# Optimization experiments

Hardware: AMD Instinct MI355X
Metric: run time of the kernel (lower is better)

The kernel has to match this reference:

```python
import jax, jax.numpy as jnp
import numpy as np

B, T, D, H = 4, 2048, 1024, 16
HD = D // H  # head_size = 64


def setup_inputs() -> dict:
    key = jax.random.key(0)
    ks = jax.random.split(key, 6)
    s = 0.02
    x = jax.random.normal(ks[0], (B, T, D), dtype=jnp.float32)
    # per-head unfused projections, stacked over heads: [H, D, HD]
    Wq = jax.random.normal(ks[1], (H, D, HD), dtype=jnp.float32) * s
    Wk = jax.random.normal(ks[2], (H, D, HD), dtype=jnp.float32) * s
    Wv = jax.random.normal(ks[3], (H, D, HD), dtype=jnp.float32) * s
    # output projection, torch Linear layout [out, in]
    Wo = jax.random.normal(ks[4], (D, D), dtype=jnp.float32) * s
    bo = jax.random.normal(ks[5], (D,), dtype=jnp.float32) * s
    return {"x": x, "Wq": Wq, "Wk": Wk, "Wv": Wv, "Wo": Wo, "bo": bo}


def reference(x, Wq, Wk, Wv, Wo, bo):
    b, t, d = x.shape
    hd = Wq.shape[-1]
    q = jnp.einsum('btd,hdk->bhtk', x, Wq)
    k = jnp.einsum('btd,hdk->bhtk', x, Wk)
    v = jnp.einsum('btd,hdk->bhtk', x, Wv)
    scores = jnp.einsum('bhtk,bhsk->bhts', q, k) / jnp.sqrt(jnp.float32(hd))
    mask = jnp.tril(jnp.ones((t, t), dtype=bool))  # causal
    scores = jnp.where(mask, scores, jnp.float32(-jnp.inf))
    p = jax.nn.softmax(scores, axis=-1)
    o = jnp.einsum('bhts,bhsk->bhtk', p, v)
    o = o.transpose(0, 2, 1, 3).reshape(b, t, d)  # concat heads
    return o @ Wo.T + bo
```

## Files before the change

kernel.cpp:

```cpp
#include <hip/hip_runtime.h>
#include <hip/hip_bf16.h>
#include <stdint.h>

#define B_   4
#define T_   2048
#define D_   1024
#define H_   16
#define HD_  64
#define MROWS (B_*T_)
#define NQKV  3072
#define NST  (T_/64)

typedef __attribute__((ext_vector_type(8))) short  short8;
typedef __attribute__((ext_vector_type(4))) short  bf16x4;
typedef __attribute__((ext_vector_type(4))) float  floatx4;

#define QSCALE 0.1803368801111244f

__device__ inline void async_copy16(const __hip_bfloat16* g, __hip_bfloat16* l) {
  __builtin_amdgcn_global_load_lds(
      (const __attribute__((address_space(1))) void*)g,
      (__attribute__((address_space(3))) void*)l, 16, 0, 0);
}

__device__ inline floatx4 mfma16(bf16x4 a, bf16x4 b, floatx4 c) {
#if __has_builtin(__builtin_amdgcn_mfma_f32_16x16x16bf16_1k)
  return __builtin_amdgcn_mfma_f32_16x16x16bf16_1k(a, b, c, 0, 0, 0);
#elif __has_builtin(__builtin_amdgcn_mfma_f32_16x16x16_bf16)
  return __builtin_amdgcn_mfma_f32_16x16x16_bf16(a, b, c, 0, 0, 0);
#else
  short8 a8 = (short8){a[0], a[1], a[2], a[3], 0, 0, 0, 0};
  short8 b8 = (short8){b[0], b[1], b[2], b[3], 0, 0, 0, 0};
  return __builtin_amdgcn_mfma_f32_16x16x32_bf16(a8, b8, c, 0, 0, 0);
#endif
}

__global__ void prep(const float* __restrict__ x, const float* __restrict__ Wo,
                     const float* __restrict__ Wq, const float* __restrict__ Wk,
                     const float* __restrict__ Wv,
                     __hip_bfloat16* __restrict__ xb, __hip_bfloat16* __restrict__ wob,
                     __hip_bfloat16* __restrict__ wqkv) {
  __shared__ __hip_bfloat16 tile[64][65];
  const int bid = (int)blockIdx.x;
  const int t = threadIdx.x;
  if (bid < 8192) {
    int i = (bid * 256 + t) * 4;
    float4 v = *(const float4*)(x + i);
    xb[i + 0] = __float2bfloat16(v.x);
    xb[i + 1] = __float2bfloat16(v.y);
    xb[i + 2] = __float2bfloat16(v.z);
    xb[i + 3] = __float2bfloat16(v.w);
  } else if (bid < 9216) {
    int i = ((bid - 8192) * 256 + t) * 4;
    float4 v = *(const float4*)(Wo + i);
    wob[i + 0] = __float2bfloat16(v.x);
    wob[i + 1] = __float2bfloat16(v.y);
    wob[i + 2] = __float2bfloat16(v.z);
    wob[i + 3] = __float2bfloat16(v.w);
  } else {
    int idx = bid - 9216;
    const int d0 = (idx & 15) * 64;
    const int wh = idx >> 4;
    const int which = wh >> 4, h = wh & 15;
    const float* W = (which == 0) ? Wq : ((which == 1) ? Wk : Wv);
    const float* base = W + (size_t)h * D_ * HD_;
#pragma unroll
    for (int i = 0; i < 16; i++) {
      int e = i * 256 + t;
      int dr = e >> 6, hd = e & 63;
      tile[dr][hd] = __float2bfloat16(base[(size_t)(d0 + dr) * HD_ + hd]);
    }
    __syncthreads();
#pragma unroll
    for (int i = 0; i < 16; i++) {
      int e = i * 256 + t;
      int hd = e >> 6, dr = e & 63;
      wqkv[(size_t)(which * 1024 + h * 64 + hd) * D_ + d0 + dr] = tile[dr][hd];
    }
  }
}

__global__ void repack_kv(const __hip_bfloat16* __restrict__ qkv,
                          __hip_bfloat16* __restrict__ kpack, __hip_bfloat16* __restrict__ vpack) {
  __shared__ __hip_bfloat16 Ks[64][72];
  __shared__ __hip_bfloat16 Vs[64][72];
  const int tid = threadIdx.x;
  const int st = blockIdx.x, bh = blockIdx.y;
  const int b = bh >> 4, h = bh & 15;
#pragma unroll
  for (int p = 0; p < 2; p++) {
    int c = p * 256 + tid;
    int row = c >> 3, col8 = c & 7;
    const __hip_bfloat16* src = qkv + (size_t)(b * T_ + st * 64 + row) * NQKV + h * HD_ + col8 * 8;
    *(uint4*)&Ks[row][col8 * 8] = *(const uint4*)(src + 1024);
    *(uint4*)&Vs[row][col8 * 8] = *(const uint4*)(src + 2048);
  }
  __syncthreads();
  const size_t base = ((size_t)bh * NST + st) * 8 * 512;
#pragma unroll
  for (int p = 0; p < 2; p++) {
    int pair = p * 256 + tid;
    int c = pair >> 6, l = pair & 63;
    int lq = l & 15, q = l >> 4;
    int ni = c >> 1, half = c & 1;
    short8 v = *(const short8*)&Ks[ni * 16 + lq][half * 32 + q * 8];
    *(short8*)(kpack + base + (size_t)c * 512 + l * 8) = v;
  }
#pragma unroll
  for (int p = 0; p < 2; p++) {
    int pair = p * 256 + tid;
    int c = pair >> 6, l = pair & 63;
    int lq = l & 15, q = l >> 4;
    int m = c >> 2, nt = c & 3;
    __hip_bfloat16 tmp[8];
#pragma unroll
    for (int half = 0; half < 2; half++)
#pragma unroll
      for (int j = 0; j < 4; j++)
        tmp[half * 4 + j] = Vs[(2 * m + half) * 16 + q * 4 + j][nt * 16 + lq];
    *(short8*)(vpack + base + (size_t)c * 512 + l * 8) = *(short8*)tmp;
  }
}

template <int EPI>
__launch_bounds__(256, 2)
__global__ void gemm_bt(const __hip_bfloat16* __restrict__ A, const __hip_bfloat16* __restrict__ Bt,
                        __hip_bfloat16* __restrict__ Cb, float* __restrict__ Cf,
                        const float* __restrict__ bias, int M, int N, int K, float qscale) {
  __shared__ __hip_bfloat16 As[128 * 32];
  __shared__ __hip_bfloat16 Bs[128 * 32];
  const int tid = threadIdx.x;
  const int w = tid >> 6, lane = tid & 63;
  const int lq = lane & 15, quad = lane >> 4;
  const int wr = w >> 1, wc = w & 1;
  const int m0 = blockIdx.x * 128, n0 = blockIdx.y * 128;

  floatx4 acc[4][4];
#pragma unroll
  for (int i = 0; i < 4; i++)
#pragma unroll
    for (int j = 0; j < 4; j++) acc[i][j] = (floatx4){0.f, 0.f, 0.f, 0.f};

  for (int k0 = 0; k0 < K; k0 += 32) {
    __syncthreads();
#pragma unroll
    for (int ph = 0; ph < 2; ++ph) {
      int c = ph * 256 + tid;
      int row = c >> 2, col8 = c & 3;
      async_copy16(A + (size_t)(m0 + row) * K + k0 + col8 * 8, As + c * 8);
      async_copy16(Bt + (size_t)(n0 + row) * K + k0 + col8 * 8, Bs + c * 8);
    }
    __syncthreads();
    short8 af[4], bf[4];
#pragma unroll
    for (int mi = 0; mi < 4; mi++)
      af[mi] = *(const short8*)(As + (wr * 64 + mi * 16 + lq) * 32 + quad * 8);
#pragma unroll
    for (int ni = 0; ni < 4; ni++)
      bf[ni] = *(const short8*)(Bs + (wc * 64 + ni * 16 + lq) * 32 + quad * 8);
#pragma unroll
    for (int mi = 0; mi < 4; mi++)
#pragma unroll
      for (int ni = 0; ni < 4; ni++)
        acc[mi][ni] = __builtin_amdgcn_mfma_f32_16x16x32_bf16(af[mi], bf[ni], acc[mi][ni], 0, 0, 0);
  }

#pragma unroll
  for (int mi = 0; mi < 4; mi++) {
#pragma unroll
    for (int ni = 0; ni < 4; ni++) {
      int col = n0 + wc * 64 + ni * 16 + lq;
      if (EPI == 0) {
        float s = (col < 1024) ? qscale : 1.0f;
#pragma unroll
        for (int r = 0; r < 4; r++) {
          int row = m0 + wr * 64 + mi * 16 + quad * 4 + r;
          Cb[(size_t)row * N + col] = __float2bfloat16(acc[mi][ni][r] * s);
        }
      } else {
        float bv = bias[col];
#pragma unroll
        for (int r = 0; r < 4; r++) {
          int row = m0 + wr * 64 + mi * 16 + quad * 4 + r;
          Cf[(size_t)row * N + col] = acc[mi][ni][r] + bv;
        }
      }
    }
  }
}

__launch_bounds__(256, 2)
__global__ void attn(const __hip_bfloat16* __restrict__ qkv,
                     const __hip_bfloat16* __restrict__ kpack,
                     const __hip_bfloat16* __restrict__ vpack,
                     __hip_bfloat16* __restrict__ obuf) {
  __shared__ __hip_bfloat16 KVs[2][8192];
  const int tid = threadIdx.x;
  const int w = tid >> 6, lane = tid & 63;
  const int lq = lane & 15, quad = lane >> 4;

  const int bh = (int)blockIdx.x;
  const int a  = (int)blockIdx.y;
  const int b = bh >> 4, h = bh & 15;

  const __hip_bfloat16* kbase = kpack + ((size_t)bh * NST) * 4096;
  const __hip_bfloat16* vbase = vpack + ((size_t)bh * NST) * 4096;

#pragma unroll 1
  for (int seg = 0; seg < 2; ++seg) {
    const int tbase = seg ? (NST - 2 - 2 * a) : (2 * a);
    const int qt = tbase + (w >> 1);
    const int rbase = (w & 1) * 32;

    short8 qf[2][2];
#pragma unroll
    for (int bi = 0; bi < 2; bi++) {
      const __hip_bfloat16* qp =
          qkv + ((size_t)(b * T_ + qt * 64 + rbase + bi * 16 + lq)) * NQKV + h * HD_;
      qf[bi][0] = *(const short8*)(qp + quad * 8);
      qf[bi][1] = *(const short8*)(qp + 32 + quad * 8);
    }

    floatx4 Oacc[2][4];
#pragma unroll
    for (int bi = 0; bi < 2; bi++)
#pragma unroll
      for (int i = 0; i < 4; i++) Oacc[bi][i] = (floatx4){0.f, 0.f, 0.f, 0.f};
    float lrow[2] = {0.f, 0.f};

    const int itTop = tbase + 1;

#pragma unroll
    for (int j = 0; j < 2; ++j) {
      int c = j * 256 + tid;
      async_copy16(kbase + (size_t)c * 8, &KVs[0][0] + c * 8);
      async_copy16(vbase + (size_t)c * 8, &KVs[0][4096] + c * 8);
    }
    __syncthreads();

#pragma unroll 1
    for (int it = 0; it <= itTop; ++it) {
      const int cur = it & 1;
      if (it < itTop) {
        const __hip_bfloat16* kn = kbase + (size_t)(it + 1) * 4096;
        const __hip_bfloat16* vn = vbase + (size_t)(it + 1) * 4096;
#pragma unroll
        for (int j = 0; j < 2; ++j) {
          int c = j * 256 + tid;
          async_copy16(kn + (size_t)c * 8, &KVs[cur ^ 1][0] + c * 8);
          async_copy16(vn + (size_t)c * 8, &KVs[cur ^ 1][4096] + c * 8);
        }
      }
      if (it <= qt) {
        const __hip_bfloat16* Kb = &KVs[cur][0] + lane * 8;
        const __hip_bfloat16* Vb = &KVs[cur][4096] + lane * 8;
        short8 kf[4], kg[4];
#pragma unroll
        for (int ni = 0; ni < 4; ni++) {
          kf[ni] = *(const short8*)(Kb + (size_t)(ni * 2 + 0) * 512);
          kg[ni] = *(const short8*)(Kb + (size_t)(ni * 2 + 1) * 512);
        }
        short8 vfr[8];
#pragma unroll
        for (int c = 0; c < 8; c++) vfr[c] = *(const short8*)(Vb + (size_t)c * 512);

        floatx4 Sc[2][4];
        __builtin_amdgcn_s_setprio(1);
#pragma unroll
        for (int bi = 0; bi < 2; bi++)
#pragma unroll
          for (int ni = 0; ni < 4; ni++) {
            floatx4 c0 = (floatx4){0.f, 0.f, 0.f, 0.f};
            c0 = __builtin_amdgcn_mfma_f32_16x16x32_bf16(kf[ni], qf[bi][0], c0, 0, 0, 0);
            c0 = __builtin_amdgcn_mfma_f32_16x16x32_bf16(kg[ni], qf[bi][1], c0, 0, 0, 0);
            Sc[bi][ni] = c0;
          }
        __builtin_amdgcn_s_setprio(0);

        if (it == qt) {
#pragma unroll
          for (int bi = 0; bi < 2; bi++) {
            int lrow_idx = rbase + bi * 16 + lq;
#pragma unroll
            for (int ni = 0; ni < 4; ni++)
#pragma unroll
              for (int r = 0; r < 4; r++) {
                int s_loc = ni * 16 + quad * 4 + r;
                if (s_loc > lrow_idx) Sc[bi][ni][r] = -__builtin_inff();
              }
          }
        }

        bf16x4 pf[2][4];
#pragma unroll
        for (int bi = 0; bi < 2; bi++)
#pragma unroll
          for (int c = 0; c < 4; c++) {
            __hip_bfloat16 pb[4];
#pragma unroll
            for (int r = 0; r < 4; r++) {
              float p = __builtin_amdgcn_exp2f(Sc[bi][c][r]);
              lrow[bi] += p;
              pb[r] = __float2bfloat16(p);
            }
            pf[bi][c] = *(bf16x4*)pb;
          }

        __builtin_amdgcn_s_setprio(1);
#pragma unroll
        for (int m = 0; m < 2; m++)
#pragma unroll
          for (int nt = 0; nt < 4; nt++) {
            short8 v8 = vfr[m * 4 + nt];
            bf16x4 vlo = (bf16x4){v8[0], v8[1], v8[2], v8[3]};
            bf16x4 vhi = (bf16x4){v8[4], v8[5], v8[6], v8[7]};
#pragma unroll
            for (int bi = 0; bi < 2; bi++) {
              Oacc[bi][nt] = mfma16(pf[bi][2 * m + 0], vlo, Oacc[bi][nt]);
              Oacc[bi][nt] = mfma16(pf[bi][2 * m + 1], vhi, Oacc[bi][nt]);
            }
          }
        __builtin_amdgcn_s_setprio(0);
      }
      __syncthreads();
    }

#pragma unroll
    for (int bi = 0; bi < 2; bi++) {
      float ps = lrow[bi];
      ps += __shfl_xor(ps, 16);
      ps += __shfl_xor(ps, 32);
      float inv = 1.0f / ps;
#pragma unroll
      for (int r = 0; r < 4; r++) {
        float invr = __shfl(inv, quad * 4 + r);
        int t = qt * 64 + rbase + bi * 16 + quad * 4 + r;
#pragma unroll
        for (int nt = 0; nt < 4; nt++)
          obuf[(size_t)(b * T_ + t) * D_ + h * HD_ + nt * 16 + lq] =
              __float2bfloat16(Oacc[bi][nt][r] * invr);
      }
    }
  }
}


extern "C" void kernel_launch(void* const* d_in, const int* in_sizes, int n_in,
                              void* d_out, int out_size, void* d_ws, size_t ws_size,
                              hipStream_t stream) {
  const float* x  = (const float*)d_in[0];
  const float* Wq = (const float*)d_in[1];
  const float* Wk = (const float*)d_in[2];
  const float* Wv = (const float*)d_in[3];
  const float* Wo = (const float*)d_in[4];
  const float* bo = (const float*)d_in[5];
  float* out = (float*)d_out;

  char* ws = (char*)d_ws;
  __hip_bfloat16* xb    = (__hip_bfloat16*)(ws);
  __hip_bfloat16* obuf  = (__hip_bfloat16*)(ws);
  __hip_bfloat16* wqkv  = (__hip_bfloat16*)(ws + ((size_t)16 << 20));
  __hip_bfloat16* wob   = (__hip_bfloat16*)(ws + ((size_t)22 << 20));
  __hip_bfloat16* qkv   = (__hip_bfloat16*)(ws + ((size_t)24 << 20));
  __hip_bfloat16* kpack = (__hip_bfloat16*)(ws + ((size_t)72 << 20));
  __hip_bfloat16* vpack = (__hip_bfloat16*)(ws + ((size_t)88 << 20));

  prep<<<9984, 256, 0, stream>>>(x, Wo, Wq, Wk, Wv, xb, wob, wqkv);

  gemm_bt<0><<<dim3(MROWS / 128, NQKV / 128), 256, 0, stream>>>(
      xb, wqkv, qkv, nullptr, nullptr, MROWS, NQKV, D_, QSCALE);

  repack_kv<<<dim3(NST, B_ * H_), 256, 0, stream>>>(qkv, kpack, vpack);

  attn<<<dim3(B_ * H_, 8), 256, 0, stream>>>(qkv, kpack, vpack, obuf);

  gemm_bt<1><<<dim3(MROWS / 128, D_ / 128), 256, 0, stream>>>(
      obuf, wob, nullptr, out, bo, MROWS, D_, D_, 1.0f);
}
```

Before: 248.7 us.

## Replace QKV projection GEMM with pipelined 128x256 tile kernel using swizzled LDS

Adds a new 512-thread GEMM for the QKV projection. It uses 128x256 output tiles with a 64-wide K step, XOR-swizzled LDS staging through async global-to-LDS loads, and double buffering that issues the next tiles' loads between the two MFMA halves. It also remaps blocks so neighbouring blocks share A/B panels in cache, and uses setprio around the MFMA bursts. The goal is to hide memory latency and cut LDS bank conflicts in the largest GEMM, at the cost of more LDS per block and a more fragile hand-tuned waitcnt/barrier schedule.

```diff
diff --git a/kernel.cpp b/kernel.cpp
--- a/kernel.cpp
+++ b/kernel.cpp
@@ -122,6 +122,128 @@
   }
 }
 
+
+__device__ inline void stage16k(const __hip_bfloat16* __restrict__ grow0, int K,
+                                short* ldst, int tid) {
+#pragma unroll
+  for (int l = 0; l < 2; ++l) {
+    int c = l * 512 + tid;
+    int r = c >> 3;
+    int sw = (c & 7) ^ (r & 7);
+    async_copy16(grow0 + (size_t)r * K + sw * 8, (__hip_bfloat16*)(ldst + c * 8));
+  }
+}
+
+__device__ inline short8 fragld2(const short* base, int r, int slot) {
+  return *(const short8*)(base + r * 64 + (((slot) ^ (r & 7)) << 3));
+}
+
+__launch_bounds__(512, 2)
+__global__ void gemmk(const __hip_bfloat16* __restrict__ A, const __hip_bfloat16* __restrict__ Bt,
+                      __hip_bfloat16* __restrict__ Cb, int M, int N, int K, float qscale) {
+  __shared__ short LDS[49152];
+  const int tid = threadIdx.x;
+  const int lane = tid & 63, wid = tid >> 6;
+  const int lq = lane & 15, quad = lane >> 4;
+  const int wr = wid >> 2, wc = wid & 3;
+
+  const int lin = (int)blockIdx.x;
+  const int s = (lin & 7) * 96 + (lin >> 3);
+  const int m0 = (s / 12) * 128, n0 = (s % 12) * 256;
+
+  const int NT = K >> 6;
+
+  floatx4 acc[4][4];
+#pragma unroll
+  for (int i = 0; i < 4; i++)
+#pragma unroll
+    for (int j = 0; j < 4; j++) acc[i][j] = (floatx4){0.f, 0.f, 0.f, 0.f};
+
+  {
+    short* b0s = LDS;
+    stage16k(A  + (size_t)m0 * K,          K, b0s,         tid);
+    stage16k(Bt + (size_t)n0 * K,          K, b0s + 8192,  tid);
+    stage16k(Bt + (size_t)(n0 + 128) * K,  K, b0s + 16384, tid);
+    short* b1s = LDS + 24576;
+    stage16k(A  + (size_t)m0 * K + 64,     K, b1s,         tid);
+    stage16k(Bt + (size_t)n0 * K + 64,     K, b1s + 8192,  tid);
+  }
+  asm volatile("s_waitcnt vmcnt(4)" ::: "memory");
+  __builtin_amdgcn_s_barrier();
+
+#pragma unroll 1
+  for (int t = 0; t < NT; ++t) {
+    short* buf = LDS + (t & 1) * 24576;
+    short* nbuf = LDS + ((t & 1) ^ 1) * 24576;
+    const int kc1 = (t + 1) << 6, kc2 = (t + 2) << 6;
+
+    short8 a[4][2], b[2][2];
+#pragma unroll
+    for (int mi = 0; mi < 4; ++mi)
+#pragma unroll
+      for (int kk = 0; kk < 2; ++kk)
+        a[mi][kk] = fragld2(buf, wr * 64 + mi * 16 + lq, kk * 4 + quad);
+#pragma unroll
+    for (int f = 0; f < 2; ++f)
+#pragma unroll
+      for (int kk = 0; kk < 2; ++kk)
+        b[f][kk] = fragld2(buf + 8192, wc * 32 + f * 16 + lq, kk * 4 + quad);
+    if (t + 1 < NT)
+      stage16k(Bt + (size_t)(n0 + 128) * K + kc1, K, nbuf + 16384, tid);
+    __builtin_amdgcn_s_barrier();
+    __builtin_amdgcn_s_setprio(1);
+#pragma unroll
+    for (int kk = 0; kk < 2; ++kk)
+#pragma unroll
+      for (int mi = 0; mi < 4; ++mi)
+#pragma unroll
+        for (int f = 0; f < 2; ++f)
+          acc[mi][f] = __builtin_amdgcn_mfma_f32_16x16x32_bf16(a[mi][kk], b[f][kk], acc[mi][f], 0, 0, 0);
+    __builtin_amdgcn_s_setprio(0);
+    __builtin_amdgcn_s_barrier();
+
+    short8 b2[2][2];
+#pragma unroll
+    for (int f = 0; f < 2; ++f)
+#pragma unroll
+      for (int kk = 0; kk < 2; ++kk)
+        b2[f][kk] = fragld2(buf + 8192, 128 + wc * 32 + f * 16 + lq, kk * 4 + quad);
+    if (t + 2 < NT) {
+      stage16k(A  + (size_t)m0 * K + kc2, K, buf,        tid);
+      stage16k(Bt + (size_t)n0 * K + kc2, K, buf + 8192, tid);
+    }
+    __builtin_amdgcn_s_barrier();
+    __builtin_amdgcn_s_setprio(1);
+#pragma unroll
+    for (int kk = 0; kk < 2; ++kk)
+#pragma unroll
+      for (int mi = 0; mi < 4; ++mi)
+#pragma unroll
+        for (int f = 0; f < 2; ++f)
+          acc[mi][2 + f] = __builtin_amdgcn_mfma_f32_16x16x32_bf16(a[mi][kk], b2[f][kk], acc[mi][2 + f], 0, 0, 0);
+    __builtin_amdgcn_s_setprio(0);
+    if (t + 2 < NT)      { asm volatile("s_waitcnt vmcnt(4)" ::: "memory"); }
+    else if (t + 1 < NT) { asm volatile("s_waitcnt vmcnt(0)" ::: "memory"); }
+    __builtin_amdgcn_s_barrier();
+  }
+
+#pragma unroll
+  for (int mi = 0; mi < 4; ++mi) {
+#pragma unroll
+    for (int nh = 0; nh < 2; ++nh)
+#pragma unroll
+      for (int f = 0; f < 2; ++f) {
+        int col = n0 + nh * 128 + wc * 32 + f * 16 + lq;
+        float sc = (col < 1024) ? qscale : 1.0f;
+#pragma unroll
+        for (int r = 0; r < 4; ++r) {
+          int row = m0 + wr * 64 + mi * 16 + quad * 4 + r;
+          Cb[(size_t)row * N + col] = __float2bfloat16(acc[mi][nh * 2 + f][r] * sc);
+        }
+      }
+  }
+}
+
 template <int EPI>
 __launch_bounds__(256, 2)
 __global__ void gemm_bt(const __hip_bfloat16* __restrict__ A, const __hip_bfloat16* __restrict__ Bt,
@@ -367,8 +489,7 @@
 
   prep<<<9984, 256, 0, stream>>>(x, Wo, Wq, Wk, Wv, xb, wob, wqkv);
 
-  gemm_bt<0><<<dim3(MROWS / 128, NQKV / 128), 256, 0, stream>>>(
-      xb, wqkv, qkv, nullptr, nullptr, MROWS, NQKV, D_, QSCALE);
+  gemmk<<<768, 512, 0, stream>>>(xb, wqkv, qkv, MROWS, NQKV, D_, QSCALE);
 
   repack_kv<<<dim3(NST, B_ * H_), 256, 0, stream>>>(qkv, kpack, vpack);
 
```

Result: slower. 257.2 us (+3.4%).
